# Kernel optimization log

Measured on AMD Instinct MI355X. Metric: run time of the kernel, lower is better.

## Reference

```python
import jax, jax.numpy as jnp
import numpy as np

HID = 1024; NH = 4; HD = HID // NH; KS = 4; C = 64; EPS = 1e-05
B = 4; L = 4096


def setup_inputs():
    key = jax.random.key(0)
    ks = jax.random.split(key, 9)
    return {
        "x": jax.random.normal(ks[0], (B, L, HID), jnp.float32),
        "Wq": jax.random.normal(ks[1], (HID, HID), jnp.float32) * 0.02,
        "Wk": jax.random.normal(ks[2], (HID, HID), jnp.float32) * 0.02,
        "Wv": jax.random.normal(ks[3], (HID, HID), jnp.float32) * 0.02,
        "Wb": jax.random.normal(ks[4], (HID, NH), jnp.float32) * 0.02,
        "conv_q": jax.random.normal(ks[5], (HID, 1, KS), jnp.float32) * 0.5,
        "conv_k": jax.random.normal(ks[6], (HID, 1, KS), jnp.float32) * 0.5,
        "conv_v": jax.random.normal(ks[7], (HID, 1, KS), jnp.float32) * 0.5,
        "g": jnp.ones((HD,), jnp.float32),
        "Wo": jax.random.normal(ks[8], (HID, HID), jnp.float32) * 0.02,
    }


def _causal_dwconv(x, w):
    # x: (B, L, Ch); w: (Ch, 1, K). Depthwise causal conv (left pad K-1) + SiLU,
    # equivalent to torch Conv1d(padding=K-1) followed by right-truncation.
    xc = jnp.moveaxis(x, 1, 2)  # (B, Ch, L)
    y = jax.lax.conv_general_dilated(
        xc, w, window_strides=(1,), padding=[(w.shape[-1] - 1, 0)],
        dimension_numbers=("NCH", "OIH", "NCH"), feature_group_count=w.shape[0])
    return jnp.moveaxis(jax.nn.silu(y), 1, 2)


def _forward(x, Wq, Wk, Wv, Wb, conv_q, conv_k, conv_v, g, Wo):
    Bx, Lx, _ = x.shape
    N = Lx // C  # num chunks (L chosen divisible by C)
    q = _causal_dwconv(x @ Wq, conv_q).reshape(Bx, Lx, NH, HD)
    k = _causal_dwconv(x @ Wk, conv_k).reshape(Bx, Lx, NH, HD)
    v = _causal_dwconv(x @ Wv, conv_v).reshape(Bx, Lx, NH, HD)
    # kq_norm: L2-normalize each head vector over head_dim
    q = q / jnp.linalg.norm(q, axis=-1, keepdims=True)
    k = k / jnp.linalg.norm(k, axis=-1, keepdims=True)
    beta = jax.nn.sigmoid(x @ Wb)  # (B, L, H)
    Q = q.reshape(Bx, N, C, NH, HD)
    K = k.reshape(Bx, N, C, NH, HD)
    V = v.reshape(Bx, N, C, NH, HD)
    bta = beta.reshape(Bx, N, C, NH, 1)
    Kb = K * bta
    Vb = V * bta
    # T = eye(C) - sum_h tril(Kb_h @ K_h^T, -1)  (T shared across heads, as in source)
    A = jnp.einsum("bnihd,bnjhd->bnij", Kb, K)
    T0 = jnp.eye(C, dtype=x.dtype) - jnp.tril(A, -1)
    col = jnp.arange(C)

    def body(i, T):
        # Replicates: T[:,:,i,:i] += (T[:,:,i,:,None] * T[:,:,:,:i]).sum(-2)
        row = jax.lax.dynamic_slice_in_dim(T, i, 1, axis=2)[:, :, 0]  # (B,N,C)
        acc = jnp.einsum("bnj,bnjc->bnc", row, T)
        new_row = jnp.where(col < i, row + acc, row)
        return jax.lax.dynamic_update_slice_in_dim(T, new_row[:, :, None, :], i, axis=2)

    T = jax.lax.fori_loop(1, C, body, T0)
    W = jnp.einsum("bnij,bnjhd->bnihd", T, Kb)
    U = jnp.einsum("bnij,bnjhd->bnihd", T, Vb)

    def chunk_step(S, inp):
        q_i, k_i, w_i, u0 = inp  # each (B, C, H, D)
        # source einsum 'bchd,bhdd->bchd' extracts the diagonal of S
        Sd = jnp.diagonal(S, axis1=-2, axis2=-1)  # (B, H, D)
        u_i = u0 - w_i * Sd[:, None]
        o_inter = q_i * Sd[:, None]
        # source: einsum('bchd,bchd->bc', q, k).tril() -- tril over the (B, C) matrix
        A_i = jnp.tril(jnp.einsum("bchd,bchd->bc", q_i, k_i))
        o_intra = A_i[:, :, None, None] * u_i
        S = S + jnp.einsum("bchd,bche->bhde", k_i, u_i)
        return S, o_inter + o_intra

    xs = tuple(jnp.moveaxis(a, 1, 0) for a in (Q, K, W, U))  # (N, B, C, H, D)
    S0 = jnp.zeros((Bx, NH, HD, HD), x.dtype)
    S, O = jax.lax.scan(chunk_step, S0, xs)
    o = jnp.moveaxis(O, 0, 1).reshape(Bx, Lx, NH, HD)
    # RMSNorm over head_dim with learned scale g
    o = o * jax.lax.rsqrt(jnp.mean(o * o, axis=-1, keepdims=True) + EPS) * g
    out = o.reshape(Bx, Lx, NH * HD) @ Wo
    return out, S


def reference(x, Wq, Wk, Wv, Wb, conv_q, conv_k, conv_v, g, Wo):
    return _forward(x, Wq, Wk, Wv, Wb, conv_q, conv_k, conv_v, g, Wo)
```

## Files before the change

kernel.cpp:

```cpp
#include <hip/hip_runtime.h>
#include <hip/hip_bf16.h>

#define HID 1024
#define NH 4
#define HD 256
#define NCH 64
#define BB 4
#define LL 4096
#define ROWS (BB*LL)
#define SSIZE (BB*NH*HD*HD)

typedef __hip_bfloat16 bf16;
typedef __attribute__((ext_vector_type(8))) short short8;
typedef __attribute__((ext_vector_type(4))) float f32x4;

struct u16x4 { unsigned short x, y, z, w; };

__device__ __forceinline__ float bfu2f(unsigned short u) {
  return __uint_as_float(((unsigned int)u) << 16);
}
__device__ __forceinline__ unsigned short f2bfu(float f) {
  unsigned int x = __float_as_uint(f);
  return (unsigned short)((x + 0x7FFFu + ((x >> 16) & 1u)) >> 16);
}
__device__ __forceinline__ float ldv(const float* p) { return *p; }
__device__ __forceinline__ float ldv(const bf16* p) { return bfu2f(*(const unsigned short*)p); }
__device__ __forceinline__ float4 ld4(const float* p) { return *(const float4*)p; }
__device__ __forceinline__ float4 ld4(const bf16* p) {
  u16x4 u = *(const u16x4*)p;
  return make_float4(bfu2f(u.x), bfu2f(u.y), bfu2f(u.z), bfu2f(u.w));
}
__device__ __forceinline__ void st4(float* p, float4 v) { *(float4*)p = v; }
__device__ __forceinline__ void st4(bf16* p, float4 v) {
  u16x4 u; u.x = f2bfu(v.x); u.y = f2bfu(v.y); u.z = f2bfu(v.z); u.w = f2bfu(v.w);
  *(u16x4*)p = u;
}
__device__ __forceinline__ void stc(float* C, size_t i, float v) { C[i] = v; }
__device__ __forceinline__ void stc(bf16* C, size_t i, float v) {
  ((unsigned short*)C)[i] = f2bfu(v);
}

typedef const __attribute__((address_space(1))) unsigned int* gptr_t;
typedef __attribute__((address_space(3))) unsigned int* lptr_t;
__device__ __forceinline__ void gload16(const void* g, void* l) {
  __builtin_amdgcn_global_load_lds((gptr_t)g, (lptr_t)l, 16, 0, 0);
}

__global__ __launch_bounds__(256)
void prep_kernel(const float* __restrict__ x, const float* __restrict__ Wb,
                 bf16* __restrict__ hi, bf16* __restrict__ lo,
                 float* __restrict__ beta) {
  const int wave = threadIdx.x >> 6, lane = threadIdx.x & 63;
  const int m = (blockIdx.x << 2) + wave;
  float a0 = 0.f, a1 = 0.f, a2 = 0.f, a3 = 0.f;
#pragma unroll
  for (int it = 0; it < 4; ++it) {
    int f4 = (it << 6) + lane;
    size_t e = (size_t)m * 256 + f4;
    float4 v = *(const float4*)&x[e << 2];
    u16x4 h; h.x = f2bfu(v.x); h.y = f2bfu(v.y); h.z = f2bfu(v.z); h.w = f2bfu(v.w);
    *(u16x4*)&hi[e << 2] = h;
    u16x4 l;
    l.x = f2bfu(v.x - bfu2f(h.x)); l.y = f2bfu(v.y - bfu2f(h.y));
    l.z = f2bfu(v.z - bfu2f(h.z)); l.w = f2bfu(v.w - bfu2f(h.w));
    *(u16x4*)&lo[e << 2] = l;
    const float xs[4] = {v.x, v.y, v.z, v.w};
#pragma unroll
    for (int j = 0; j < 4; ++j) {
      float4 wb = *(const float4*)&Wb[((f4 << 2) + j) << 2];
      a0 += xs[j] * wb.x; a1 += xs[j] * wb.y;
      a2 += xs[j] * wb.z; a3 += xs[j] * wb.w;
    }
  }
#pragma unroll
  for (int off = 32; off; off >>= 1) {
    a0 += __shfl_xor(a0, off); a1 += __shfl_xor(a1, off);
    a2 += __shfl_xor(a2, off); a3 += __shfl_xor(a3, off);
  }
  if (lane == 0) {
    float4 r;
    r.x = 1.f / (1.f + expf(-a0)); r.y = 1.f / (1.f + expf(-a1));
    r.z = 1.f / (1.f + expf(-a2)); r.w = 1.f / (1.f + expf(-a3));
    *(float4*)&beta[m << 2] = r;
  }
}

__global__ __launch_bounds__(256)
void convT_all(const float* __restrict__ Wq, const float* __restrict__ Wv,
               const float* __restrict__ Wo, const float* __restrict__ Wk,
               unsigned short* __restrict__ Wqt, unsigned short* __restrict__ Wvt,
               unsigned short* __restrict__ Wot, unsigned short* __restrict__ Wkht,
               unsigned short* __restrict__ Wklt) {
  __shared__ float t[64][65];
  const int z = blockIdx.z;
  const float* W = z == 0 ? Wq : z == 1 ? Wv : z == 2 ? Wo : Wk;
  const int kt = blockIdx.x << 6, nt = blockIdx.y << 6;
  const int tid = threadIdx.x;
#pragma unroll
  for (int i = 0; i < 16; ++i) {
    int idx = tid + (i << 8);
    int r = idx >> 6, c = idx & 63;
    t[r][c] = W[(size_t)(kt + r) * HID + nt + c];
  }
  __syncthreads();
  if (z < 3) {
    unsigned short* Wt = z == 0 ? Wqt : z == 1 ? Wvt : Wot;
#pragma unroll
    for (int i = 0; i < 16; ++i) {
      int idx = tid + (i << 8);
      int n = idx >> 6, kk = idx & 63;
      Wt[(size_t)(nt + n) * HID + kt + kk] = f2bfu(t[kk][n]);
    }
  } else {
#pragma unroll
    for (int i = 0; i < 16; ++i) {
      int idx = tid + (i << 8);
      int n = idx >> 6, kk = idx & 63;
      float v = t[kk][n];
      unsigned short h = f2bfu(v);
      Wkht[(size_t)(nt + n) * HID + kt + kk] = h;
      Wklt[(size_t)(nt + n) * HID + kt + kk] = f2bfu(v - bfu2f(h));
    }
  }
}

__global__ __launch_bounds__(256)
void ktrans_kernel(const float* __restrict__ k, unsigned short* __restrict__ kt) {
  __shared__ float t[64][65];
  const int r0 = blockIdx.x << 6, c0 = blockIdx.y << 6;
  const int tid = threadIdx.x;
#pragma unroll
  for (int i = 0; i < 16; ++i) {
    int idx = tid + (i << 8);
    int rr = idx >> 6, cc = idx & 63;
    t[rr][cc] = k[(size_t)(r0 + rr) * HID + c0 + cc];
  }
  __syncthreads();
#pragma unroll
  for (int i = 0; i < 16; ++i) {
    int idx = tid + (i << 8);
    int cc = idx >> 6, rr = idx & 63;
    kt[(size_t)(c0 + cc) * ROWS + r0 + rr] = f2bfu(t[rr][cc]);
  }
}

template <typename OT>
__global__ __launch_bounds__(256)
void mfma_gemm(const unsigned short* __restrict__ A,
               const unsigned short* __restrict__ Bt, OT* __restrict__ C) {
  __shared__ unsigned short Asl[128 * 32];
  __shared__ unsigned short Bsl[128 * 32];
  const int tid = threadIdx.x;
  const int wave = tid >> 6, lane = tid & 63;
  const int m0 = blockIdx.x << 7, n0 = blockIdx.y << 7;
  const int wr = wave >> 1, wc = wave & 1;
  f32x4 acc[4][4] = {};
  const int cA = (wave << 6) + lane;
  for (int k0 = 0; k0 < HID; k0 += 32) {
#pragma unroll
    for (int i = 0; i < 2; ++i) {
      int c = cA + (i << 8);
      int row = c >> 2, ko = (c & 3) << 3;
      gload16(&A[(size_t)(m0 + row) * HID + k0 + ko],
              &Asl[(size_t)((i << 8) + (wave << 6)) * 8]);
      gload16(&Bt[(size_t)(n0 + row) * HID + k0 + ko],
              &Bsl[(size_t)((i << 8) + (wave << 6)) * 8]);
    }
    __syncthreads();
    short8 af[4], bfr[4];
#pragma unroll
    for (int f = 0; f < 4; ++f) {
      int ra = (wr << 6) + (f << 4) + (lane & 15);
      af[f] = *(const short8*)&Asl[ra * 32 + ((lane >> 4) << 3)];
      int rb = (wc << 6) + (f << 4) + (lane & 15);
      bfr[f] = *(const short8*)&Bsl[rb * 32 + ((lane >> 4) << 3)];
    }
#pragma unroll
    for (int i = 0; i < 4; ++i)
#pragma unroll
      for (int j = 0; j < 4; ++j)
        acc[i][j] = __builtin_amdgcn_mfma_f32_16x16x32_bf16(af[i], bfr[j],
                                                            acc[i][j], 0, 0, 0);
    __syncthreads();
  }
#pragma unroll
  for (int i = 0; i < 4; ++i) {
    int r0 = m0 + (wr << 6) + (i << 4) + ((lane >> 4) << 2);
#pragma unroll
    for (int j = 0; j < 4; ++j) {
      int c0 = n0 + (wc << 6) + (j << 4) + (lane & 15);
#pragma unroll
      for (int r = 0; r < 4; ++r)
        stc(C, (size_t)(r0 + r) * HID + c0, acc[i][j][r]);
    }
  }
}

__global__ __launch_bounds__(256)
void mfma_gemm3(const unsigned short* __restrict__ Ah_,
                const unsigned short* __restrict__ Al_,
                const unsigned short* __restrict__ Bh_,
                const unsigned short* __restrict__ Bl_,
                float* __restrict__ C) {
  __shared__ unsigned short Ah[128 * 32];
  __shared__ unsigned short Al[128 * 32];
  __shared__ unsigned short Bh[128 * 32];
  __shared__ unsigned short Bl[128 * 32];
  const int tid = threadIdx.x;
  const int wave = tid >> 6, lane = tid & 63;
  const int m0 = blockIdx.x << 7, n0 = blockIdx.y << 7;
  const int wr = wave >> 1, wc = wave & 1;
  f32x4 acc[4][4] = {};
  const int cA = (wave << 6) + lane;
  for (int k0 = 0; k0 < HID; k0 += 32) {
#pragma unroll
    for (int i = 0; i < 2; ++i) {
      int c = cA + (i << 8);
      int row = c >> 2, ko = (c & 3) << 3;
      size_t ga = (size_t)(m0 + row) * HID + k0 + ko;
      size_t gb = (size_t)(n0 + row) * HID + k0 + ko;
      size_t ldst = (size_t)((i << 8) + (wave << 6)) * 8;
      gload16(&Ah_[ga], &Ah[ldst]);
      gload16(&Al_[ga], &Al[ldst]);
      gload16(&Bh_[gb], &Bh[ldst]);
      gload16(&Bl_[gb], &Bl[ldst]);
    }
    __syncthreads();
    short8 ah[4], al[4], bh[4], bl[4];
#pragma unroll
    for (int f = 0; f < 4; ++f) {
      int ra = ((wr << 6) + (f << 4) + (lane & 15)) * 32 + ((lane >> 4) << 3);
      ah[f] = *(const short8*)&Ah[ra];
      al[f] = *(const short8*)&Al[ra];
      int rb = ((wc << 6) + (f << 4) + (lane & 15)) * 32 + ((lane >> 4) << 3);
      bh[f] = *(const short8*)&Bh[rb];
      bl[f] = *(const short8*)&Bl[rb];
    }
#pragma unroll
    for (int i = 0; i < 4; ++i)
#pragma unroll
      for (int j = 0; j < 4; ++j) {
        f32x4 a = acc[i][j];
        a = __builtin_amdgcn_mfma_f32_16x16x32_bf16(al[i], bh[j], a, 0, 0, 0);
        a = __builtin_amdgcn_mfma_f32_16x16x32_bf16(ah[i], bl[j], a, 0, 0, 0);
        a = __builtin_amdgcn_mfma_f32_16x16x32_bf16(ah[i], bh[j], a, 0, 0, 0);
        acc[i][j] = a;
      }
    __syncthreads();
  }
#pragma unroll
  for (int i = 0; i < 4; ++i) {
    int r0 = m0 + (wr << 6) + (i << 4) + ((lane >> 4) << 2);
#pragma unroll
    for (int j = 0; j < 4; ++j) {
      int c0 = n0 + (wc << 6) + (j << 4) + (lane & 15);
#pragma unroll
      for (int r = 0; r < 4; ++r)
        C[(size_t)(r0 + r) * HID + c0] = acc[i][j][r];
    }
  }
}

__global__ __launch_bounds__(256)
void mfma_gemmS(const unsigned short* __restrict__ At,
                const unsigned short* __restrict__ Bt,
                float* __restrict__ Spart, int ngroups) {
  __shared__ unsigned short Asl[128 * 32];
  __shared__ unsigned short Bsl[128 * 32];
  const int tid = threadIdx.x;
  const int wave = tid >> 6, lane = tid & 63;
  const int m0 = blockIdx.x << 7, n0 = blockIdx.y << 7;
  const int bh = blockIdx.z / ngroups;
  const int ng = blockIdx.z % ngroups;
  const int b = bh >> 2, h = bh & 3;
  const size_t kbase = (size_t)b * LL + (size_t)ng * (LL / ngroups);
  const int wr = wave >> 1, wc = wave & 1;
  f32x4 acc[4][4] = {};
  const int cA = (wave << 6) + lane;
  for (int k0 = 0; k0 < LL / ngroups; k0 += 32) {
#pragma unroll
    for (int i = 0; i < 2; ++i) {
      int c = cA + (i << 8);
      int row = c >> 2, ko = (c & 3) << 3;
      gload16(&At[((size_t)(h * HD + m0 + row)) * ROWS + kbase + k0 + ko],
              &Asl[(size_t)((i << 8) + (wave << 6)) * 8]);
      gload16(&Bt[((size_t)(bh * HD + n0 + row)) * LL + (size_t)ng * (LL / ngroups) + k0 + ko],
              &Bsl[(size_t)((i << 8) + (wave << 6)) * 8]);
    }
    __syncthreads();
    short8 af[4], bfr[4];
#pragma unroll
    for (int f = 0; f < 4; ++f) {
      int ra = (wr << 6) + (f << 4) + (lane & 15);
      af[f] = *(const short8*)&Asl[ra * 32 + ((lane >> 4) << 3)];
      int rb = (wc << 6) + (f << 4) + (lane & 15);
      bfr[f] = *(const short8*)&Bsl[rb * 32 + ((lane >> 4) << 3)];
    }
#pragma unroll
    for (int i = 0; i < 4; ++i)
#pragma unroll
      for (int j = 0; j < 4; ++j)
        acc[i][j] = __builtin_amdgcn_mfma_f32_16x16x32_bf16(af[i], bfr[j],
                                                            acc[i][j], 0, 0, 0);
    __syncthreads();
  }
  float* Cp = Spart + (size_t)ng * SSIZE + (size_t)bh * HD * HD;
#pragma unroll
  for (int i = 0; i < 4; ++i) {
    int r0 = m0 + (wr << 6) + (i << 4) + ((lane >> 4) << 2);
#pragma unroll
    for (int j = 0; j < 4; ++j) {
      int c0 = n0 + (wc << 6) + (j << 4) + (lane & 15);
#pragma unroll
      for (int r = 0; r < 4; ++r)
        Cp[(size_t)(r0 + r) * HD + c0] = acc[i][j][r];
    }
  }
}

template <int MODE, typename IT, typename ST>
__global__ __launch_bounds__(256)
void conv8_kernel(const IT* __restrict__ lin, const float* __restrict__ w,
                  const float* __restrict__ beta, ST* __restrict__ out) {
  const int row0 = blockIdx.x << 3;
  const int tid = threadIdx.x;
  const int ch = tid << 2;
  const int h = tid >> 6;
  float wv[4][4];
#pragma unroll
  for (int j = 0; j < 4; ++j) {
    float4 t4 = *(const float4*)&w[(ch + j) << 2];
    wv[j][0] = t4.x; wv[j][1] = t4.y; wv[j][2] = t4.z; wv[j][3] = t4.w;
  }
  const int l0 = row0 & (LL - 1);
  const bool hasprev = (l0 != 0);
  float4 xw0, xw1, xw2, xw3;
  const float4 z4 = make_float4(0.f, 0.f, 0.f, 0.f);
  xw0 = hasprev ? ld4(&lin[(size_t)(row0 - 3) * HID + ch]) : z4;
  xw1 = hasprev ? ld4(&lin[(size_t)(row0 - 2) * HID + ch]) : z4;
  xw2 = hasprev ? ld4(&lin[(size_t)(row0 - 1) * HID + ch]) : z4;
#pragma unroll
  for (int r = 0; r < 8; ++r) {
    const int gr = row0 + r;
    xw3 = ld4(&lin[(size_t)gr * HID + ch]);
    float y[4];
#pragma unroll
    for (int j = 0; j < 4; ++j) {
      float xv0 = j == 0 ? xw0.x : j == 1 ? xw0.y : j == 2 ? xw0.z : xw0.w;
      float xv1 = j == 0 ? xw1.x : j == 1 ? xw1.y : j == 2 ? xw1.z : xw1.w;
      float xv2 = j == 0 ? xw2.x : j == 1 ? xw2.y : j == 2 ? xw2.z : xw2.w;
      float xv3 = j == 0 ? xw3.x : j == 1 ? xw3.y : j == 2 ? xw3.z : xw3.w;
      y[j] = xv0 * wv[j][0] + xv1 * wv[j][1] + xv2 * wv[j][2] + xv3 * wv[j][3];
      y[j] = y[j] / (1.f + expf(-y[j]));
    }
    float scale;
    if (MODE < 2) {
      float ss = y[0]*y[0] + y[1]*y[1] + y[2]*y[2] + y[3]*y[3];
#pragma unroll
      for (int off = 32; off; off >>= 1) ss += __shfl_xor(ss, off);
      scale = 1.f / sqrtf(ss);
    } else {
      scale = beta[(gr << 2) + h];
    }
    st4(&out[(size_t)gr * HID + ch],
        make_float4(y[0]*scale, y[1]*scale, y[2]*scale, y[3]*scale));
    xw0 = xw1; xw1 = xw2; xw2 = xw3;
  }
}

__global__ __launch_bounds__(256)
void chunkT_kernel(const float* __restrict__ k, const float* __restrict__ beta,
                   float* __restrict__ Tg) {
  __shared__ float T[64][68];
  __shared__ float S1[64][68];
  __shared__ float S2[64][68];
  __shared__ float row_s[64];
  const int bn = blockIdx.x;
  const size_t base = (size_t)bn * 64 * HID;
  const int tid = threadIdx.x;
  const int tr = tid >> 4, tc = tid & 15;
  float acc[4][4] = {{0.f}};
  for (int d0 = 0; d0 < HID; d0 += 64) {
    const int h = d0 >> 8;
#pragma unroll
    for (int p = 0; p < 4; ++p) {
      int rr = (tid >> 4) + (p << 4);
      int c4 = (tid & 15) << 2;
      float4 a = *(const float4*)&k[base + (size_t)rr * HID + d0 + c4];
      float bta = beta[(((bn << 6) + rr) << 2) + h];
      S2[c4 + 0][rr] = a.x; S2[c4 + 1][rr] = a.y;
      S2[c4 + 2][rr] = a.z; S2[c4 + 3][rr] = a.w;
      S1[c4 + 0][rr] = a.x * bta; S1[c4 + 1][rr] = a.y * bta;
      S1[c4 + 2][rr] = a.z * bta; S1[c4 + 3][rr] = a.w * bta;
    }
    __syncthreads();
#pragma unroll
    for (int dd = 0; dd < 64; ++dd) {
      float4 a = *(const float4*)&S1[dd][tr << 2];
      float4 b = *(const float4*)&S2[dd][tc << 2];
      acc[0][0] += a.x*b.x; acc[0][1] += a.x*b.y; acc[0][2] += a.x*b.z; acc[0][3] += a.x*b.w;
      acc[1][0] += a.y*b.x; acc[1][1] += a.y*b.y; acc[1][2] += a.y*b.z; acc[1][3] += a.y*b.w;
      acc[2][0] += a.z*b.x; acc[2][1] += a.z*b.y; acc[2][2] += a.z*b.z; acc[2][3] += a.z*b.w;
      acc[3][0] += a.w*b.x; acc[3][1] += a.w*b.y; acc[3][2] += a.w*b.z; acc[3][3] += a.w*b.w;
    }
    __syncthreads();
  }
#pragma unroll
  for (int i = 0; i < 4; ++i)
#pragma unroll
    for (int j = 0; j < 4; ++j) {
      int ri = (tr << 2) + i, cj = (tc << 2) + j;
      T[ri][cj] = (ri == cj) ? 1.f : (ri > cj ? -acc[i][j] : 0.f);
    }
  __syncthreads();
  for (int i = 1; i < 64; ++i) {
    if (tid < 64) row_s[tid] = T[i][tid];
    __syncthreads();
    if (tid < 64) {
      float a = 0.f;
#pragma unroll 8
      for (int j = 0; j < 64; ++j) a += row_s[j] * T[j][tid];
      if (tid < i) T[i][tid] = row_s[tid] + a;
    }
    __syncthreads();
  }
#pragma unroll
  for (int ii = 0; ii < 4; ++ii) {
    int off = (tid << 4) + (ii << 2);
    int c = off >> 6, j = off & 63;
    *(float4*)&Tg[(size_t)bn * 4096 + off] = *(const float4*)&T[c][j];
  }
}

template <typename ST>
__global__ __launch_bounds__(256)
void prct_kernel(const float* __restrict__ k, const ST* __restrict__ v,
                 const float* __restrict__ beta, const float* __restrict__ Tg,
                 float* __restrict__ P, float* __restrict__ R) {
  __shared__ float Ts[4096];
  __shared__ float bs[64];
  const int bn = blockIdx.x >> 2, h = blockIdx.x & 3;
  const int tid = threadIdx.x;
#pragma unroll
  for (int ii = 0; ii < 4; ++ii) {
    int off = (tid << 4) + (ii << 2);
    *(float4*)&Ts[off] = *(const float4*)&Tg[(size_t)bn * 4096 + off];
  }
  if (tid < 64) bs[tid] = beta[(((bn << 6) + tid) << 2) + h];
  __syncthreads();
  const int ch = (h << 8) + tid;
  const size_t base = (size_t)bn * 64 * HID;
  float ct[64];
#pragma unroll
  for (int j = 0; j < 64; ++j) ct[j] = 0.f;
  for (int c = 0; c < 64; ++c) {
    float kc = k[base + (size_t)c * HID + ch];
#pragma unroll
    for (int j = 0; j < 64; ++j) ct[j] += Ts[(c << 6) + j] * kc;
  }
  float p = 0.f, r = 0.f;
#pragma unroll
  for (int j = 0; j < 64; ++j) {
    float kj = k[base + (size_t)j * HID + ch];
    float vj = ldv(&v[base + (size_t)j * HID + ch]);
    p += bs[j] * kj * ct[j];
    r += vj * ct[j];
  }
  P[(size_t)bn * HID + ch] = p;
  R[(size_t)bn * HID + ch] = r;
}

__global__ __launch_bounds__(256)
void scan_kernel(const float* __restrict__ P, const float* __restrict__ R,
                 float* __restrict__ Sdp) {
  const int b = blockIdx.x >> 2;
  const int ch = ((blockIdx.x & 3) << 8) + threadIdx.x;
  float S = 0.f;
  for (int n = 0; n < 64; ++n) {
    Sdp[(size_t)((n << 2) + b) * HID + ch] = S;
    float p = P[(size_t)((b << 6) + n) * HID + ch];
    float r = R[(size_t)((b << 6) + n) * HID + ch];
    S = S * (1.f - p) + r;
  }
}

template <typename ST>
__global__ __launch_bounds__(256)
void ai_kernel(const ST* __restrict__ q, const float* __restrict__ k,
               float* __restrict__ Ai) {
  const int bn = blockIdx.x;
  const int b = bn >> 6;
  const int wave = threadIdx.x >> 6, lane = threadIdx.x & 63;
  const size_t roff = ((size_t)bn * 64 + wave) * HID;
  float s = 0.f;
#pragma unroll
  for (int it = 0; it < 4; ++it) {
    int d = (lane << 2) + (it << 8);
    float4 a = ld4(&q[roff + d]);
    float4 b4 = *(const float4*)&k[roff + d];
    s += a.x*b4.x + a.y*b4.y + a.z*b4.z + a.w*b4.w;
  }
#pragma unroll
  for (int off = 32; off; off >>= 1) s += __shfl_xor(s, off);
  if (lane == 0) Ai[(bn << 2) + wave] = (wave <= b) ? s : 0.f;
}

__global__ __launch_bounds__(256)
void ucompute_kernel(const float* __restrict__ k, const bf16* __restrict__ v,
                     const float* __restrict__ beta, const float* __restrict__ Tg,
                     const float* __restrict__ Sdp, unsigned short* __restrict__ Ut) {
  __shared__ float Ts[4096];
  __shared__ float va[64][132];
  __shared__ float bs[64];
  const int bn = blockIdx.x >> 3;
  const int rr2 = blockIdx.x & 7;
  const int h = rr2 >> 1, eh = rr2 & 1;
  const int b = bn >> 6, nl = bn & 63;
  const int tid = threadIdx.x;
#pragma unroll
  for (int ii = 0; ii < 4; ++ii) {
    int off = (tid << 4) + (ii << 2);
    *(float4*)&Ts[off] = *(const float4*)&Tg[(size_t)bn * 4096 + off];
  }
  if (tid < 64) bs[tid] = beta[(((bn << 6) + tid) << 2) + h];
  __syncthreads();
  const size_t base = (size_t)bn * 64 * HID;
  const int ch0 = (h << 8) + (eh << 7);
#pragma unroll
  for (int p = 0; p < 8; ++p) {
    int idx = tid + (p << 8);
    int row = idx >> 5;
    int col4 = (idx & 31) << 2;
    int chg = ch0 + col4;
    float4 sd4 = *(const float4*)&Sdp[(size_t)((nl << 2) + b) * HID + chg];
    float4 k4 = *(const float4*)&k[base + (size_t)row * HID + chg];
    float4 v4 = ld4(&v[base + (size_t)row * HID + chg]);
    float bt = bs[row];
    va[row][col4 + 0] = v4.x - bt * k4.x * sd4.x;
    va[row][col4 + 1] = v4.y - bt * k4.y * sd4.y;
    va[row][col4 + 2] = v4.z - bt * k4.z * sd4.z;
    va[row][col4 + 3] = v4.w - bt * k4.w * sd4.w;
  }
  __syncthreads();
  const int e = tid & 127;
  const int chalf = tid >> 7;
  float acc[32];
#pragma unroll
  for (int c2 = 0; c2 < 32; ++c2) acc[c2] = 0.f;
  for (int j = 0; j < 64; ++j) {
    float vaj = va[j][e];
#pragma unroll
    for (int c2 = 0; c2 < 32; ++c2)
      acc[c2] += Ts[((chalf << 5) + c2) * 64 + j] * vaj;
  }
  const size_t ub = ((size_t)(((b << 2) + h) * HD) + (eh << 7) + e) * LL
                  + (nl << 6) + (chalf << 5);
#pragma unroll
  for (int c4 = 0; c4 < 8; ++c4) {
    u16x4 u;
    u.x = f2bfu(acc[(c4 << 2) + 0]); u.y = f2bfu(acc[(c4 << 2) + 1]);
    u.z = f2bfu(acc[(c4 << 2) + 2]); u.w = f2bfu(acc[(c4 << 2) + 3]);
    *(u16x4*)&Ut[ub + (c4 << 2)] = u;
  }
}

template <typename ST>
__global__ __launch_bounds__(256)
void o_kernel(ST* __restrict__ q, const float* __restrict__ Sdp,
              const unsigned short* __restrict__ Ut, const float* __restrict__ Ai,
              const float* __restrict__ g) {
  const int row = blockIdx.x;
  const int b = row >> 12;
  const int l = row & (LL - 1);
  const int n = l >> 6, c = l & 63;
  const int ch = threadIdx.x << 2;
  const size_t ro = (size_t)row * HID;
  float4 qv = ld4(&q[ro + ch]);
  float4 sd = *(const float4*)&Sdp[(size_t)((n << 2) + b) * HID + ch];
  float ox = qv.x*sd.x, oy = qv.y*sd.y, oz = qv.z*sd.z, ow = qv.w*sd.w;
  if (c <= b) {
    int bn = (b << 6) + n;
    float a = Ai[(bn << 2) + c];
    const int h = ch >> 8, e = ch & 255;
    const size_t ub = ((size_t)(((b << 2) + h) * HD) + e) * LL + (n << 6) + c;
    ox += a * bfu2f(Ut[ub + 0 * LL]);
    oy += a * bfu2f(Ut[ub + 1 * LL]);
    oz += a * bfu2f(Ut[ub + 2 * LL]);
    ow += a * bfu2f(Ut[ub + 3 * LL]);
  }
  float ss = ox*ox + oy*oy + oz*oz + ow*ow;
#pragma unroll
  for (int off = 32; off; off >>= 1) ss += __shfl_xor(ss, off);
  float scale = 1.f / sqrtf(ss * (1.f / HD) + 1e-5f);
  float4 gv = *(const float4*)&g[ch & (HD - 1)];
  st4(&q[ro + ch], make_float4(ox*scale*gv.x, oy*scale*gv.y, oz*scale*gv.z, ow*scale*gv.w));
}

__global__ __launch_bounds__(256)
void sreduce_kernel(const float* __restrict__ Spart, float* __restrict__ Sout,
                    int ngroups) {
  size_t i = ((size_t)blockIdx.x * 256 + threadIdx.x) << 2;
  float4 s = make_float4(0.f, 0.f, 0.f, 0.f);
  for (int g = 0; g < ngroups; ++g) {
    float4 p = *(const float4*)&Spart[(size_t)g * SSIZE + i];
    s.x += p.x; s.y += p.y; s.z += p.z; s.w += p.w;
  }
  *(float4*)&Sout[i] = s;
}

extern "C" void kernel_launch(void* const* d_in, const int* in_sizes, int n_in,
                              void* d_out, int out_size, void* d_ws, size_t ws_size,
                              hipStream_t stream) {
  const float* x  = (const float*)d_in[0];
  const float* Wq = (const float*)d_in[1];
  const float* Wk = (const float*)d_in[2];
  const float* Wv = (const float*)d_in[3];
  const float* Wb = (const float*)d_in[4];
  const float* cq = (const float*)d_in[5];
  const float* ck = (const float*)d_in[6];
  const float* cv = (const float*)d_in[7];
  const float* g  = (const float*)d_in[8];
  const float* Wo = (const float*)d_in[9];
  float* out  = (float*)d_out;
  float* Sout = out + (size_t)ROWS * HID;

  const size_t F = (size_t)ROWS * HID;
  char* w = (char*)d_ws;
  float* kbuf  = (float*)w;  w += F * 4;
  bf16*  xb    = (bf16*)w;   w += F * 2;
  bf16*  qbuf  = (bf16*)w;   w += F * 2;
  bf16*  vbuf  = (bf16*)w;   w += F * 2;
  unsigned short* Wqt  = (unsigned short*)w; w += (size_t)HID * HID * 2;
  unsigned short* Wvt  = (unsigned short*)w; w += (size_t)HID * HID * 2;
  unsigned short* Wot  = (unsigned short*)w; w += (size_t)HID * HID * 2;
  unsigned short* Wkht = (unsigned short*)w; w += (size_t)HID * HID * 2;
  unsigned short* Wklt = (unsigned short*)w; w += (size_t)HID * HID * 2;
  float* Tg    = (float*)w;  w += (size_t)BB * NCH * 4096 * 4;
  float* betab = (float*)w;  w += (size_t)ROWS * NH * 4;
  float* Aib   = (float*)w;  w += (size_t)BB * NCH * 4 * 4;
  float* Pb    = (float*)w;  w += (size_t)BB * NCH * HID * 4;
  float* Rb    = (float*)w;  w += (size_t)BB * NCH * HID * 4;
  float* Sdp   = (float*)w;  w += (size_t)BB * NCH * HID * 4;
  const size_t need = (size_t)(w - (char*)d_ws);
  if (ws_size < need) return;

  dim3 gg(ROWS / 128, HID / 128);
  float* linf = out;
  bf16*  linb = (bf16*)out;
  bf16*  xlo  = qbuf;

  prep_kernel<<<ROWS / 4, 256, 0, stream>>>(x, Wb, xb, xlo, betab);
  convT_all<<<dim3(16, 16, 4), 256, 0, stream>>>(Wq, Wv, Wo, Wk, Wqt, Wvt, Wot,
                                                 Wkht, Wklt);

  mfma_gemm3<<<gg, 256, 0, stream>>>((const unsigned short*)xb,
                                     (const unsigned short*)xlo, Wkht, Wklt, linf);
  conv8_kernel<1, float, float><<<ROWS / 8, 256, 0, stream>>>(linf, ck, betab, kbuf);
  mfma_gemm<bf16><<<gg, 256, 0, stream>>>((const unsigned short*)xb, Wqt, linb);
  conv8_kernel<0, bf16, bf16><<<ROWS / 8, 256, 0, stream>>>(linb, cq, betab, qbuf);
  mfma_gemm<bf16><<<gg, 256, 0, stream>>>((const unsigned short*)xb, Wvt, linb);
  conv8_kernel<2, bf16, bf16><<<ROWS / 8, 256, 0, stream>>>(linb, cv, betab, vbuf);

  unsigned short* kt = (unsigned short*)xb;
  ktrans_kernel<<<dim3(ROWS / 64, HID / 64), 256, 0, stream>>>(kbuf, kt);

  chunkT_kernel<<<BB * NCH, 256, 0, stream>>>(kbuf, betab, Tg);
  prct_kernel<bf16><<<BB * NCH * NH, 256, 0, stream>>>(kbuf, vbuf, betab, Tg, Pb, Rb);
  scan_kernel<<<16, 256, 0, stream>>>(Pb, Rb, Sdp);
  ai_kernel<bf16><<<BB * NCH, 256, 0, stream>>>(qbuf, kbuf, Aib);

  unsigned short* Ut = (unsigned short*)linb;
  ucompute_kernel<<<BB * NCH * NH * 2, 256, 0, stream>>>(kbuf, vbuf, betab, Tg,
                                                         Sdp, Ut);
  o_kernel<bf16><<<ROWS, 256, 0, stream>>>(qbuf, Sdp, Ut, Aib, g);

  float* Spart = kbuf;
  const int ngroups = 8;
  mfma_gemmS<<<dim3(2, 2, 16 * ngroups), 256, 0, stream>>>(kt, Ut, Spart, ngroups);
  sreduce_kernel<<<SSIZE / 1024, 256, 0, stream>>>(Spart, Sout, ngroups);

  mfma_gemm<float><<<gg, 256, 0, stream>>>((const unsigned short*)qbuf, Wot, out);
}
```

Before: 706.0 us.

## Merge independent kernels into combined launches to cut launch count

```diff
diff --git a/kernel.cpp b/kernel.cpp
--- a/kernel.cpp
+++ b/kernel.cpp
@@ -46,113 +46,14 @@
   __builtin_amdgcn_global_load_lds((gptr_t)g, (lptr_t)l, 16, 0, 0);
 }
 
-__global__ __launch_bounds__(256)
-void prep_kernel(const float* __restrict__ x, const float* __restrict__ Wb,
-                 bf16* __restrict__ hi, bf16* __restrict__ lo,
-                 float* __restrict__ beta) {
-  const int wave = threadIdx.x >> 6, lane = threadIdx.x & 63;
-  const int m = (blockIdx.x << 2) + wave;
-  float a0 = 0.f, a1 = 0.f, a2 = 0.f, a3 = 0.f;
-#pragma unroll
-  for (int it = 0; it < 4; ++it) {
-    int f4 = (it << 6) + lane;
-    size_t e = (size_t)m * 256 + f4;
-    float4 v = *(const float4*)&x[e << 2];
-    u16x4 h; h.x = f2bfu(v.x); h.y = f2bfu(v.y); h.z = f2bfu(v.z); h.w = f2bfu(v.w);
-    *(u16x4*)&hi[e << 2] = h;
-    u16x4 l;
-    l.x = f2bfu(v.x - bfu2f(h.x)); l.y = f2bfu(v.y - bfu2f(h.y));
-    l.z = f2bfu(v.z - bfu2f(h.z)); l.w = f2bfu(v.w - bfu2f(h.w));
-    *(u16x4*)&lo[e << 2] = l;
-    const float xs[4] = {v.x, v.y, v.z, v.w};
-#pragma unroll
-    for (int j = 0; j < 4; ++j) {
-      float4 wb = *(const float4*)&Wb[((f4 << 2) + j) << 2];
-      a0 += xs[j] * wb.x; a1 += xs[j] * wb.y;
-      a2 += xs[j] * wb.z; a3 += xs[j] * wb.w;
-    }
-  }
-#pragma unroll
-  for (int off = 32; off; off >>= 1) {
-    a0 += __shfl_xor(a0, off); a1 += __shfl_xor(a1, off);
-    a2 += __shfl_xor(a2, off); a3 += __shfl_xor(a3, off);
-  }
-  if (lane == 0) {
-    float4 r;
-    r.x = 1.f / (1.f + expf(-a0)); r.y = 1.f / (1.f + expf(-a1));
-    r.z = 1.f / (1.f + expf(-a2)); r.w = 1.f / (1.f + expf(-a3));
-    *(float4*)&beta[m << 2] = r;
-  }
-}
-
-__global__ __launch_bounds__(256)
-void convT_all(const float* __restrict__ Wq, const float* __restrict__ Wv,
-               const float* __restrict__ Wo, const float* __restrict__ Wk,
-               unsigned short* __restrict__ Wqt, unsigned short* __restrict__ Wvt,
-               unsigned short* __restrict__ Wot, unsigned short* __restrict__ Wkht,
-               unsigned short* __restrict__ Wklt) {
-  __shared__ float t[64][65];
-  const int z = blockIdx.z;
-  const float* W = z == 0 ? Wq : z == 1 ? Wv : z == 2 ? Wo : Wk;
-  const int kt = blockIdx.x << 6, nt = blockIdx.y << 6;
-  const int tid = threadIdx.x;
-#pragma unroll
-  for (int i = 0; i < 16; ++i) {
-    int idx = tid + (i << 8);
-    int r = idx >> 6, c = idx & 63;
-    t[r][c] = W[(size_t)(kt + r) * HID + nt + c];
-  }
-  __syncthreads();
-  if (z < 3) {
-    unsigned short* Wt = z == 0 ? Wqt : z == 1 ? Wvt : Wot;
-#pragma unroll
-    for (int i = 0; i < 16; ++i) {
-      int idx = tid + (i << 8);
-      int n = idx >> 6, kk = idx & 63;
-      Wt[(size_t)(nt + n) * HID + kt + kk] = f2bfu(t[kk][n]);
-    }
-  } else {
-#pragma unroll
-    for (int i = 0; i < 16; ++i) {
-      int idx = tid + (i << 8);
-      int n = idx >> 6, kk = idx & 63;
-      float v = t[kk][n];
-      unsigned short h = f2bfu(v);
-      Wkht[(size_t)(nt + n) * HID + kt + kk] = h;
-      Wklt[(size_t)(nt + n) * HID + kt + kk] = f2bfu(v - bfu2f(h));
-    }
-  }
-}
-
-__global__ __launch_bounds__(256)
-void ktrans_kernel(const float* __restrict__ k, unsigned short* __restrict__ kt) {
-  __shared__ float t[64][65];
-  const int r0 = blockIdx.x << 6, c0 = blockIdx.y << 6;
-  const int tid = threadIdx.x;
-#pragma unroll
-  for (int i = 0; i < 16; ++i) {
-    int idx = tid + (i << 8);
-    int rr = idx >> 6, cc = idx & 63;
-    t[rr][cc] = k[(size_t)(r0 + rr) * HID + c0 + cc];
-  }
-  __syncthreads();
-#pragma unroll
-  for (int i = 0; i < 16; ++i) {
-    int idx = tid + (i << 8);
-    int cc = idx >> 6, rr = idx & 63;
-    kt[(size_t)(c0 + cc) * ROWS + r0 + rr] = f2bfu(t[rr][cc]);
-  }
-}
 
 template <typename OT>
-__global__ __launch_bounds__(256)
-void mfma_gemm(const unsigned short* __restrict__ A,
-               const unsigned short* __restrict__ Bt, OT* __restrict__ C) {
-  __shared__ unsigned short Asl[128 * 32];
-  __shared__ unsigned short Bsl[128 * 32];
+__device__ __forceinline__
+void gemm_body(const unsigned short* __restrict__ A,
+               const unsigned short* __restrict__ Bt, OT* __restrict__ C,
+               int m0, int n0, unsigned short* Asl, unsigned short* Bsl) {
   const int tid = threadIdx.x;
   const int wave = tid >> 6, lane = tid & 63;
-  const int m0 = blockIdx.x << 7, n0 = blockIdx.y << 7;
   const int wr = wave >> 1, wc = wave & 1;
   f32x4 acc[4][4] = {};
   const int cA = (wave << 6) + lane;
@@ -192,6 +93,137 @@
 #pragma unroll
       for (int r = 0; r < 4; ++r)
         stc(C, (size_t)(r0 + r) * HID + c0, acc[i][j][r]);
+    }
+  }
+}
+
+template <int MODE, typename IT, typename ST>
+__device__ __forceinline__
+void conv8_body(const IT* __restrict__ lin, const float* __restrict__ w,
+                const float* __restrict__ beta, ST* __restrict__ out, int row0) {
+  const int tid = threadIdx.x;
+  const int ch = tid << 2;
+  const int h = tid >> 6;
+  float wv[4][4];
+#pragma unroll
+  for (int j = 0; j < 4; ++j) {
+    float4 t4 = *(const float4*)&w[(ch + j) << 2];
+    wv[j][0] = t4.x; wv[j][1] = t4.y; wv[j][2] = t4.z; wv[j][3] = t4.w;
+  }
+  const int l0 = row0 & (LL - 1);
+  const bool hasprev = (l0 != 0);
+  float4 xw0, xw1, xw2, xw3;
+  const float4 z4 = make_float4(0.f, 0.f, 0.f, 0.f);
+  xw0 = hasprev ? ld4(&lin[(size_t)(row0 - 3) * HID + ch]) : z4;
+  xw1 = hasprev ? ld4(&lin[(size_t)(row0 - 2) * HID + ch]) : z4;
+  xw2 = hasprev ? ld4(&lin[(size_t)(row0 - 1) * HID + ch]) : z4;
+#pragma unroll
+  for (int r = 0; r < 8; ++r) {
+    const int gr = row0 + r;
+    xw3 = ld4(&lin[(size_t)gr * HID + ch]);
+    float y[4];
+#pragma unroll
+    for (int j = 0; j < 4; ++j) {
+      float xv0 = j == 0 ? xw0.x : j == 1 ? xw0.y : j == 2 ? xw0.z : xw0.w;
+      float xv1 = j == 0 ? xw1.x : j == 1 ? xw1.y : j == 2 ? xw1.z : xw1.w;
+      float xv2 = j == 0 ? xw2.x : j == 1 ? xw2.y : j == 2 ? xw2.z : xw2.w;
+      float xv3 = j == 0 ? xw3.x : j == 1 ? xw3.y : j == 2 ? xw3.z : xw3.w;
+      y[j] = xv0 * wv[j][0] + xv1 * wv[j][1] + xv2 * wv[j][2] + xv3 * wv[j][3];
+      y[j] = y[j] / (1.f + expf(-y[j]));
+    }
+    float scale;
+    if (MODE < 2) {
+      float ss = y[0]*y[0] + y[1]*y[1] + y[2]*y[2] + y[3]*y[3];
+#pragma unroll
+      for (int off = 32; off; off >>= 1) ss += __shfl_xor(ss, off);
+      scale = 1.f / sqrtf(ss);
+    } else {
+      scale = beta[(gr << 2) + h];
+    }
+    st4(&out[(size_t)gr * HID + ch],
+        make_float4(y[0]*scale, y[1]*scale, y[2]*scale, y[3]*scale));
+    xw0 = xw1; xw1 = xw2; xw2 = xw3;
+  }
+}
+
+
+__global__ __launch_bounds__(256)
+void prep_convT(const float* __restrict__ x, const float* __restrict__ Wb,
+                const float* __restrict__ Wq, const float* __restrict__ Wv,
+                const float* __restrict__ Wo, const float* __restrict__ Wk,
+                bf16* __restrict__ hi, bf16* __restrict__ lo,
+                float* __restrict__ beta,
+                unsigned short* __restrict__ Wqt, unsigned short* __restrict__ Wvt,
+                unsigned short* __restrict__ Wot, unsigned short* __restrict__ Wkht,
+                unsigned short* __restrict__ Wklt) {
+  __shared__ float t[64][65];
+  const int bx = blockIdx.x;
+  const int tid = threadIdx.x;
+  if (bx < 4096) {
+    const int wave = tid >> 6, lane = tid & 63;
+    const int m = (bx << 2) + wave;
+    float a0 = 0.f, a1 = 0.f, a2 = 0.f, a3 = 0.f;
+#pragma unroll
+    for (int it = 0; it < 4; ++it) {
+      int f4 = (it << 6) + lane;
+      size_t e = (size_t)m * 256 + f4;
+      float4 v = *(const float4*)&x[e << 2];
+      u16x4 h; h.x = f2bfu(v.x); h.y = f2bfu(v.y); h.z = f2bfu(v.z); h.w = f2bfu(v.w);
+      *(u16x4*)&hi[e << 2] = h;
+      u16x4 l;
+      l.x = f2bfu(v.x - bfu2f(h.x)); l.y = f2bfu(v.y - bfu2f(h.y));
+      l.z = f2bfu(v.z - bfu2f(h.z)); l.w = f2bfu(v.w - bfu2f(h.w));
+      *(u16x4*)&lo[e << 2] = l;
+      const float xs[4] = {v.x, v.y, v.z, v.w};
+#pragma unroll
+      for (int j = 0; j < 4; ++j) {
+        float4 wb = *(const float4*)&Wb[((f4 << 2) + j) << 2];
+        a0 += xs[j] * wb.x; a1 += xs[j] * wb.y;
+        a2 += xs[j] * wb.z; a3 += xs[j] * wb.w;
+      }
+    }
+#pragma unroll
+    for (int off = 32; off; off >>= 1) {
+      a0 += __shfl_xor(a0, off); a1 += __shfl_xor(a1, off);
+      a2 += __shfl_xor(a2, off); a3 += __shfl_xor(a3, off);
+    }
+    if (lane == 0) {
+      float4 r;
+      r.x = 1.f / (1.f + expf(-a0)); r.y = 1.f / (1.f + expf(-a1));
+      r.z = 1.f / (1.f + expf(-a2)); r.w = 1.f / (1.f + expf(-a3));
+      *(float4*)&beta[m << 2] = r;
+    }
+  } else {
+    const int idx = bx - 4096;
+    const int z = idx >> 8;
+    const int xy = idx & 255;
+    const int kt = (xy & 15) << 6, nt = (xy >> 4) << 6;
+    const float* W = z == 0 ? Wq : z == 1 ? Wv : z == 2 ? Wo : Wk;
+#pragma unroll
+    for (int i = 0; i < 16; ++i) {
+      int id2 = tid + (i << 8);
+      int r = id2 >> 6, c = id2 & 63;
+      t[r][c] = W[(size_t)(kt + r) * HID + nt + c];
+    }
+    __syncthreads();
+    if (z < 3) {
+      unsigned short* Wt = z == 0 ? Wqt : z == 1 ? Wvt : Wot;
+#pragma unroll
+      for (int i = 0; i < 16; ++i) {
+        int id2 = tid + (i << 8);
+        int n = id2 >> 6, kk = id2 & 63;
+        Wt[(size_t)(nt + n) * HID + kt + kk] = f2bfu(t[kk][n]);
+      }
+    } else {
+#pragma unroll
+      for (int i = 0; i < 16; ++i) {
+        int id2 = tid + (i << 8);
+        int n = id2 >> 6, kk = id2 & 63;
+        float v = t[kk][n];
+        unsigned short h = f2bfu(v);
+        Wkht[(size_t)(nt + n) * HID + kt + kk] = h;
+        Wklt[(size_t)(nt + n) * HID + kt + kk] = f2bfu(v - bfu2f(h));
+      }
     }
   }
 }
@@ -262,109 +294,52 @@
 }
 
 __global__ __launch_bounds__(256)
-void mfma_gemmS(const unsigned short* __restrict__ At,
-                const unsigned short* __restrict__ Bt,
-                float* __restrict__ Spart, int ngroups) {
+void conv8_k(const float* __restrict__ lin, const float* __restrict__ w,
+             const float* __restrict__ beta, float* __restrict__ out) {
+  conv8_body<1, float, float>(lin, w, beta, out, blockIdx.x << 3);
+}
+
+__global__ __launch_bounds__(256)
+void qv_gemm(const unsigned short* __restrict__ A,
+             const unsigned short* __restrict__ Wqt,
+             const unsigned short* __restrict__ Wvt,
+             bf16* __restrict__ linq, bf16* __restrict__ linv) {
   __shared__ unsigned short Asl[128 * 32];
   __shared__ unsigned short Bsl[128 * 32];
-  const int tid = threadIdx.x;
-  const int wave = tid >> 6, lane = tid & 63;
-  const int m0 = blockIdx.x << 7, n0 = blockIdx.y << 7;
-  const int bh = blockIdx.z / ngroups;
-  const int ng = blockIdx.z % ngroups;
-  const int b = bh >> 2, h = bh & 3;
-  const size_t kbase = (size_t)b * LL + (size_t)ng * (LL / ngroups);
-  const int wr = wave >> 1, wc = wave & 1;
-  f32x4 acc[4][4] = {};
-  const int cA = (wave << 6) + lane;
-  for (int k0 = 0; k0 < LL / ngroups; k0 += 32) {
-#pragma unroll
-    for (int i = 0; i < 2; ++i) {
-      int c = cA + (i << 8);
-      int row = c >> 2, ko = (c & 3) << 3;
-      gload16(&At[((size_t)(h * HD + m0 + row)) * ROWS + kbase + k0 + ko],
-              &Asl[(size_t)((i << 8) + (wave << 6)) * 8]);
-      gload16(&Bt[((size_t)(bh * HD + n0 + row)) * LL + (size_t)ng * (LL / ngroups) + k0 + ko],
-              &Bsl[(size_t)((i << 8) + (wave << 6)) * 8]);
-    }
-    __syncthreads();
-    short8 af[4], bfr[4];
-#pragma unroll
-    for (int f = 0; f < 4; ++f) {
-      int ra = (wr << 6) + (f << 4) + (lane & 15);
-      af[f] = *(const short8*)&Asl[ra * 32 + ((lane >> 4) << 3)];
-      int rb = (wc << 6) + (f << 4) + (lane & 15);
-      bfr[f] = *(const short8*)&Bsl[rb * 32 + ((lane >> 4) << 3)];
-    }
-#pragma unroll
-    for (int i = 0; i < 4; ++i)
-#pragma unroll
-      for (int j = 0; j < 4; ++j)
-        acc[i][j] = __builtin_amdgcn_mfma_f32_16x16x32_bf16(af[i], bfr[j],
-                                                            acc[i][j], 0, 0, 0);
-    __syncthreads();
-  }
-  float* Cp = Spart + (size_t)ng * SSIZE + (size_t)bh * HD * HD;
-#pragma unroll
-  for (int i = 0; i < 4; ++i) {
-    int r0 = m0 + (wr << 6) + (i << 4) + ((lane >> 4) << 2);
-#pragma unroll
-    for (int j = 0; j < 4; ++j) {
-      int c0 = n0 + (wc << 6) + (j << 4) + (lane & 15);
-#pragma unroll
-      for (int r = 0; r < 4; ++r)
-        Cp[(size_t)(r0 + r) * HD + c0] = acc[i][j][r];
-    }
-  }
-}
-
-template <int MODE, typename IT, typename ST>
-__global__ __launch_bounds__(256)
-void conv8_kernel(const IT* __restrict__ lin, const float* __restrict__ w,
-                  const float* __restrict__ beta, ST* __restrict__ out) {
-  const int row0 = blockIdx.x << 3;
-  const int tid = threadIdx.x;
-  const int ch = tid << 2;
-  const int h = tid >> 6;
-  float wv[4][4];
-#pragma unroll
-  for (int j = 0; j < 4; ++j) {
-    float4 t4 = *(const float4*)&w[(ch + j) << 2];
-    wv[j][0] = t4.x; wv[j][1] = t4.y; wv[j][2] = t4.z; wv[j][3] = t4.w;
-  }
-  const int l0 = row0 & (LL - 1);
-  const bool hasprev = (l0 != 0);
-  float4 xw0, xw1, xw2, xw3;
-  const float4 z4 = make_float4(0.f, 0.f, 0.f, 0.f);
-  xw0 = hasprev ? ld4(&lin[(size_t)(row0 - 3) * HID + ch]) : z4;
-  xw1 = hasprev ? ld4(&lin[(size_t)(row0 - 2) * HID + ch]) : z4;
-  xw2 = hasprev ? ld4(&lin[(size_t)(row0 - 1) * HID + ch]) : z4;
-#pragma unroll
-  for (int r = 0; r < 8; ++r) {
-    const int gr = row0 + r;
-    xw3 = ld4(&lin[(size_t)gr * HID + ch]);
-    float y[4];
-#pragma unroll
-    for (int j = 0; j < 4; ++j) {
-      float xv0 = j == 0 ? xw0.x : j == 1 ? xw0.y : j == 2 ? xw0.z : xw0.w;
-      float xv1 = j == 0 ? xw1.x : j == 1 ? xw1.y : j == 2 ? xw1.z : xw1.w;
-      float xv2 = j == 0 ? xw2.x : j == 1 ? xw2.y : j == 2 ? xw2.z : xw2.w;
-      float xv3 = j == 0 ? xw3.x : j == 1 ? xw3.y : j == 2 ? xw3.z : xw3.w;
-      y[j] = xv0 * wv[j][0] + xv1 * wv[j][1] + xv2 * wv[j][2] + xv3 * wv[j][3];
-      y[j] = y[j] / (1.f + expf(-y[j]));
-    }
-    float scale;
-    if (MODE < 2) {
-      float ss = y[0]*y[0] + y[1]*y[1] + y[2]*y[2] + y[3]*y[3];
-#pragma unroll
-      for (int off = 32; off; off >>= 1) ss += __shfl_xor(ss, off);
-      scale = 1.f / sqrtf(ss);
-    } else {
-      scale = beta[(gr << 2) + h];
-    }
-    st4(&out[(size_t)gr * HID + ch],
-        make_float4(y[0]*scale, y[1]*scale, y[2]*scale, y[3]*scale));
-    xw0 = xw1; xw1 = xw2; xw2 = xw3;
+  const unsigned short* Bt = blockIdx.z ? Wvt : Wqt;
+  bf16* C = blockIdx.z ? linv : linq;
+  gemm_body<bf16>(A, Bt, C, blockIdx.x << 7, blockIdx.y << 7, Asl, Bsl);
+}
+
+__global__ __launch_bounds__(256)
+void convqv_ktrans(const bf16* __restrict__ linq, const bf16* __restrict__ linv,
+                   const float* __restrict__ cq, const float* __restrict__ cv,
+                   const float* __restrict__ beta, bf16* __restrict__ qbuf,
+                   bf16* __restrict__ vbuf, const float* __restrict__ k,
+                   unsigned short* __restrict__ kt) {
+  __shared__ float t[64][65];
+  const int bx = blockIdx.x;
+  if (bx < 2048) {
+    conv8_body<0, bf16, bf16>(linq, cq, beta, qbuf, bx << 3);
+  } else if (bx < 4096) {
+    conv8_body<2, bf16, bf16>(linv, cv, beta, vbuf, (bx - 2048) << 3);
+  } else {
+    const int idx = bx - 4096;
+    const int r0 = (idx & 255) << 6, c0 = (idx >> 8) << 6;
+    const int tid = threadIdx.x;
+#pragma unroll
+    for (int i = 0; i < 16; ++i) {
+      int id2 = tid + (i << 8);
+      int rr = id2 >> 6, cc = id2 & 63;
+      t[rr][cc] = k[(size_t)(r0 + rr) * HID + c0 + cc];
+    }
+    __syncthreads();
+#pragma unroll
+    for (int i = 0; i < 16; ++i) {
+      int id2 = tid + (i << 8);
+      int cc = id2 >> 6, rr = id2 & 63;
+      kt[(size_t)(c0 + cc) * ROWS + r0 + rr] = f2bfu(t[rr][cc]);
+    }
   }
 }
 
@@ -432,9 +407,8 @@
   }
 }
 
-template <typename ST>
-__global__ __launch_bounds__(256)
-void prct_kernel(const float* __restrict__ k, const ST* __restrict__ v,
+__global__ __launch_bounds__(256)
+void prct_kernel(const float* __restrict__ k, const bf16* __restrict__ v,
                  const float* __restrict__ beta, const float* __restrict__ Tg,
                  float* __restrict__ P, float* __restrict__ R) {
   __shared__ float Ts[4096];
@@ -471,38 +445,43 @@
 }
 
 __global__ __launch_bounds__(256)
-void scan_kernel(const float* __restrict__ P, const float* __restrict__ R,
-                 float* __restrict__ Sdp) {
-  const int b = blockIdx.x >> 2;
-  const int ch = ((blockIdx.x & 3) << 8) + threadIdx.x;
-  float S = 0.f;
-  for (int n = 0; n < 64; ++n) {
-    Sdp[(size_t)((n << 2) + b) * HID + ch] = S;
-    float p = P[(size_t)((b << 6) + n) * HID + ch];
-    float r = R[(size_t)((b << 6) + n) * HID + ch];
-    S = S * (1.f - p) + r;
-  }
-}
-
-template <typename ST>
-__global__ __launch_bounds__(256)
-void ai_kernel(const ST* __restrict__ q, const float* __restrict__ k,
-               float* __restrict__ Ai) {
-  const int bn = blockIdx.x;
-  const int b = bn >> 6;
-  const int wave = threadIdx.x >> 6, lane = threadIdx.x & 63;
-  const size_t roff = ((size_t)bn * 64 + wave) * HID;
-  float s = 0.f;
-#pragma unroll
-  for (int it = 0; it < 4; ++it) {
-    int d = (lane << 2) + (it << 8);
-    float4 a = ld4(&q[roff + d]);
-    float4 b4 = *(const float4*)&k[roff + d];
-    s += a.x*b4.x + a.y*b4.y + a.z*b4.z + a.w*b4.w;
-  }
-#pragma unroll
-  for (int off = 32; off; off >>= 1) s += __shfl_xor(s, off);
-  if (lane == 0) Ai[(bn << 2) + wave] = (wave <= b) ? s : 0.f;
+void scan_ai(const float* __restrict__ P, const float* __restrict__ R,
+             float* __restrict__ Sdp, const bf16* __restrict__ q,
+             const float* __restrict__ k, float* __restrict__ Ai) {
+  const int bx = blockIdx.x;
+  if (bx < 16) {
+    const int b = bx >> 2;
+    const int ch = ((bx & 3) << 8) + threadIdx.x;
+    float S = 0.f;
+    float p = P[(size_t)(b << 6) * HID + ch];
+    float r = R[(size_t)(b << 6) * HID + ch];
+    for (int n = 0; n < 64; ++n) {
+      Sdp[(size_t)((n << 2) + b) * HID + ch] = S;
+      float pn = 0.f, rn = 0.f;
+      if (n < 63) {
+        pn = P[(size_t)((b << 6) + n + 1) * HID + ch];
+        rn = R[(size_t)((b << 6) + n + 1) * HID + ch];
+      }
+      S = S * (1.f - p) + r;
+      p = pn; r = rn;
+    }
+  } else {
+    const int bn = bx - 16;
+    const int b = bn >> 6;
+    const int wave = threadIdx.x >> 6, lane = threadIdx.x & 63;
+    const size_t roff = ((size_t)bn * 64 + wave) * HID;
+    float s = 0.f;
+#pragma unroll
+    for (int it = 0; it < 4; ++it) {
+      int d = (lane << 2) + (it << 8);
+      float4 a = ld4(&q[roff + d]);
+      float4 b4 = *(const float4*)&k[roff + d];
+      s += a.x*b4.x + a.y*b4.y + a.z*b4.z + a.w*b4.w;
+    }
+#pragma unroll
+    for (int off = 32; off; off >>= 1) s += __shfl_xor(s, off);
+    if (lane == 0) Ai[(bn << 2) + wave] = (wave <= b) ? s : 0.f;
+  }
 }
 
 __global__ __launch_bounds__(256)
@@ -564,9 +543,8 @@
   }
 }
 
-template <typename ST>
-__global__ __launch_bounds__(256)
-void o_kernel(ST* __restrict__ q, const float* __restrict__ Sdp,
+__global__ __launch_bounds__(256)
+void o_kernel(bf16* __restrict__ q, const float* __restrict__ Sdp,
               const unsigned short* __restrict__ Ut, const float* __restrict__ Ai,
               const float* __restrict__ g) {
   const int row = blockIdx.x;
@@ -597,15 +575,81 @@
 }
 
 __global__ __launch_bounds__(256)
-void sreduce_kernel(const float* __restrict__ Spart, float* __restrict__ Sout,
-                    int ngroups) {
-  size_t i = ((size_t)blockIdx.x * 256 + threadIdx.x) << 2;
-  float4 s = make_float4(0.f, 0.f, 0.f, 0.f);
-  for (int g = 0; g < ngroups; ++g) {
-    float4 p = *(const float4*)&Spart[(size_t)g * SSIZE + i];
-    s.x += p.x; s.y += p.y; s.z += p.z; s.w += p.w;
-  }
-  *(float4*)&Sout[i] = s;
+void mfma_gemmS(const unsigned short* __restrict__ At,
+                const unsigned short* __restrict__ Bt,
+                float* __restrict__ Spart, int ngroups) {
+  __shared__ unsigned short Asl[128 * 32];
+  __shared__ unsigned short Bsl[128 * 32];
+  const int tid = threadIdx.x;
+  const int wave = tid >> 6, lane = tid & 63;
+  const int m0 = blockIdx.x << 7, n0 = blockIdx.y << 7;
+  const int bh = blockIdx.z / ngroups;
+  const int ng = blockIdx.z % ngroups;
+  const int b = bh >> 2, h = bh & 3;
+  const size_t kbase = (size_t)b * LL + (size_t)ng * (LL / ngroups);
+  const int wr = wave >> 1, wc = wave & 1;
+  f32x4 acc[4][4] = {};
+  const int cA = (wave << 6) + lane;
+  for (int k0 = 0; k0 < LL / ngroups; k0 += 32) {
+#pragma unroll
+    for (int i = 0; i < 2; ++i) {
+      int c = cA + (i << 8);
+      int row = c >> 2, ko = (c & 3) << 3;
+      gload16(&At[((size_t)(h * HD + m0 + row)) * ROWS + kbase + k0 + ko],
+              &Asl[(size_t)((i << 8) + (wave << 6)) * 8]);
+      gload16(&Bt[((size_t)(bh * HD + n0 + row)) * LL + (size_t)ng * (LL / ngroups) + k0 + ko],
+              &Bsl[(size_t)((i << 8) + (wave << 6)) * 8]);
+    }
+    __syncthreads();
+    short8 af[4], bfr[4];
+#pragma unroll
+    for (int f = 0; f < 4; ++f) {
+      int ra = (wr << 6) + (f << 4) + (lane & 15);
+      af[f] = *(const short8*)&Asl[ra * 32 + ((lane >> 4) << 3)];
+      int rb = (wc << 6) + (f << 4) + (lane & 15);
+      bfr[f] = *(const short8*)&Bsl[rb * 32 + ((lane >> 4) << 3)];
+    }
+#pragma unroll
+    for (int i = 0; i < 4; ++i)
+#pragma unroll
+      for (int j = 0; j < 4; ++j)
+        acc[i][j] = __builtin_amdgcn_mfma_f32_16x16x32_bf16(af[i], bfr[j],
+                                                            acc[i][j], 0, 0, 0);
+    __syncthreads();
+  }
+  float* Cp = Spart + (size_t)ng * SSIZE + (size_t)bh * HD * HD;
+#pragma unroll
+  for (int i = 0; i < 4; ++i) {
+    int r0 = m0 + (wr << 6) + (i << 4) + ((lane >> 4) << 2);
+#pragma unroll
+    for (int j = 0; j < 4; ++j) {
+      int c0 = n0 + (wc << 6) + (j << 4) + (lane & 15);
+#pragma unroll
+      for (int r = 0; r < 4; ++r)
+        Cp[(size_t)(r0 + r) * HD + c0] = acc[i][j][r];
+    }
+  }
+}
+
+__global__ __launch_bounds__(256)
+void out_sreduce(const unsigned short* __restrict__ A,
+                 const unsigned short* __restrict__ Bt, float* __restrict__ C,
+                 const float* __restrict__ Spart, float* __restrict__ Sout,
+                 int ngroups) {
+  __shared__ unsigned short Asl[128 * 32];
+  __shared__ unsigned short Bsl[128 * 32];
+  const int bx = blockIdx.x;
+  if (bx < 1024) {
+    gemm_body<float>(A, Bt, C, (bx >> 3) << 7, (bx & 7) << 7, Asl, Bsl);
+  } else {
+    size_t i = ((size_t)(bx - 1024) * 256 + threadIdx.x) << 2;
+    float4 s = make_float4(0.f, 0.f, 0.f, 0.f);
+    for (int g = 0; g < ngroups; ++g) {
+      float4 p = *(const float4*)&Spart[(size_t)g * SSIZE + i];
+      s.x += p.x; s.y += p.y; s.z += p.z; s.w += p.w;
+    }
+    *(float4*)&Sout[i] = s;
+  }
 }
 
 extern "C" void kernel_launch(void* const* d_in, const int* in_sizes, int n_in,
@@ -646,38 +690,31 @@
 
   dim3 gg(ROWS / 128, HID / 128);
   float* linf = out;
-  bf16*  linb = (bf16*)out;
+  bf16*  linq = (bf16*)out;
+  bf16*  linv = linq + F;
   bf16*  xlo  = qbuf;
 
-  prep_kernel<<<ROWS / 4, 256, 0, stream>>>(x, Wb, xb, xlo, betab);
-  convT_all<<<dim3(16, 16, 4), 256, 0, stream>>>(Wq, Wv, Wo, Wk, Wqt, Wvt, Wot,
-                                                 Wkht, Wklt);
-
+  prep_convT<<<4096 + 1024, 256, 0, stream>>>(x, Wb, Wq, Wv, Wo, Wk, xb, xlo,
+                                              betab, Wqt, Wvt, Wot, Wkht, Wklt);
   mfma_gemm3<<<gg, 256, 0, stream>>>((const unsigned short*)xb,
                                      (const unsigned short*)xlo, Wkht, Wklt, linf);
-  conv8_kernel<1, float, float><<<ROWS / 8, 256, 0, stream>>>(linf, ck, betab, kbuf);
-  mfma_gemm<bf16><<<gg, 256, 0, stream>>>((const unsigned short*)xb, Wqt, linb);
-  conv8_kernel<0, bf16, bf16><<<ROWS / 8, 256, 0, stream>>>(linb, cq, betab, qbuf);
-  mfma_gemm<bf16><<<gg, 256, 0, stream>>>((const unsigned short*)xb, Wvt, linb);
-  conv8_kernel<2, bf16, bf16><<<ROWS / 8, 256, 0, stream>>>(linb, cv, betab, vbuf);
-
+  conv8_k<<<ROWS / 8, 256, 0, stream>>>(linf, ck, betab, kbuf);
+  qv_gemm<<<dim3(ROWS / 128, HID / 128, 2), 256, 0, stream>>>(
+      (const unsigned short*)xb, Wqt, Wvt, linq, linv);
   unsigned short* kt = (unsigned short*)xb;
-  ktrans_kernel<<<dim3(ROWS / 64, HID / 64), 256, 0, stream>>>(kbuf, kt);
-
+  convqv_ktrans<<<2048 + 2048 + 4096, 256, 0, stream>>>(linq, linv, cq, cv,
+                                                        betab, qbuf, vbuf,
+                                                        kbuf, kt);
   chunkT_kernel<<<BB * NCH, 256, 0, stream>>>(kbuf, betab, Tg);
-  prct_kernel<bf16><<<BB * NCH * NH, 256, 0, stream>>>(kbuf, vbuf, betab, Tg, Pb, Rb);
-  scan_kernel<<<16, 256, 0, stream>>>(Pb, Rb, Sdp);
-  ai_kernel<bf16><<<BB * NCH, 256, 0, stream>>>(qbuf, kbuf, Aib);
-
-  unsigned short* Ut = (unsigned short*)linb;
+  prct_kernel<<<BB * NCH * NH, 256, 0, stream>>>(kbuf, vbuf, betab, Tg, Pb, Rb);
+  scan_ai<<<16 + BB * NCH, 256, 0, stream>>>(Pb, Rb, Sdp, qbuf, kbuf, Aib);
+  unsigned short* Ut = (unsigned short*)out;
   ucompute_kernel<<<BB * NCH * NH * 2, 256, 0, stream>>>(kbuf, vbuf, betab, Tg,
                                                          Sdp, Ut);
-  o_kernel<bf16><<<ROWS, 256, 0, stream>>>(qbuf, Sdp, Ut, Aib, g);
-
+  o_kernel<<<ROWS, 256, 0, stream>>>(qbuf, Sdp, Ut, Aib, g);
   float* Spart = kbuf;
   const int ngroups = 8;
   mfma_gemmS<<<dim3(2, 2, 16 * ngroups), 256, 0, stream>>>(kt, Ut, Spart, ngroups);
-  sreduce_kernel<<<SSIZE / 1024, 256, 0, stream>>>(Spart, Sout, ngroups);
-
-  mfma_gemm<float><<<gg, 256, 0, stream>>>((const unsigned short*)qbuf, Wot, out);
-}
+  out_sreduce<<<1024 + SSIZE / 1024, 256, 0, stream>>>(
+      (const unsigned short*)qbuf, Wot, out, Spart, Sout, ngroups);
+}
```

Measured after the change: 678.7 us. 1.04x faster.
